# Performance work log

Hardware: AMD Instinct MI355X
Metric: run time of the kernel (lower is better)

Reference implementation:

```python
import jax, jax.numpy as jnp
import numpy as np

UP_TIME = 1440.0
UP_DIST = 40.0
LOC_CNT = 100000
LOC_LEN = 131072
H = 256


def setup_inputs() -> dict:
    key = jax.random.key(0)
    ks = jax.random.split(key, 12)
    stdv = 1.0 / np.sqrt(H)
    u = lambda k, shape: jax.random.uniform(k, shape, jnp.float32, -stdv, stdv)
    return {
        "td_upper": jax.random.uniform(ks[0], (LOC_LEN,), jnp.float32),
        "td_lower": jax.random.uniform(ks[1], (LOC_LEN,), jnp.float32),
        "ld_upper": jax.random.uniform(ks[2], (LOC_LEN,), jnp.float32),
        "ld_lower": jax.random.uniform(ks[3], (LOC_LEN,), jnp.float32),
        "loc": jax.random.randint(ks[4], (LOC_LEN,), 0, LOC_CNT, jnp.int32),
        "hx": jax.random.normal(ks[5], (H, 1), jnp.float32),
        "weight_ih": u(ks[6], (H, H)),
        "weight_th_upper": u(ks[7], (H, H)),
        "weight_th_lower": u(ks[8], (H, H)),
        "weight_sh_upper": u(ks[9], (H, H)),
        "weight_sh_lower": u(ks[10], (H, H)),
        "location_weight": u(ks[11], (LOC_CNT, H)),
    }


def reference(td_upper, td_lower, ld_upper, ld_lower, loc, hx,
              weight_ih, weight_th_upper, weight_th_lower,
              weight_sh_upper, weight_sh_lower, location_weight):
    tu = jnp.clip(td_upper, 0.0, UP_TIME)
    tl = jnp.clip(td_lower, 0.0, UP_TIME)
    lu = jnp.clip(ld_upper, 0.0, UP_DIST)
    ll = jnp.clip(ld_lower, 0.0, UP_DIST)

    e = location_weight[loc]  # [L, H] gathered POI embeddings
    # Ttd[i] @ e[i] = (tu[i]*W_tu@e[i] + tl[i]*W_tl@e[i]) / (tu[i]+tl[i])
    a = jnp.einsum('hk,lk->lh', weight_th_upper, e)
    b = jnp.einsum('hk,lk->lh', weight_th_lower, e)
    t = (tu[:, None] * a + tl[:, None] * b) / (tu + tl)[:, None]  # [L, H]
    # Sld[i] @ t[i]
    c = jnp.einsum('hk,lk->lh', weight_sh_upper, t)
    d = jnp.einsum('hk,lk->lh', weight_sh_lower, t)
    s = (lu[:, None] * c + ll[:, None] * d) / (lu + ll)[:, None]  # [L, H]

    loc_vec = jnp.sum(s, axis=0)[:, None]  # [H, 1]
    usr_vec = weight_ih @ hx               # [H, 1]
    return jax.nn.sigmoid(loc_vec + usr_vec)
```

## Files before the change

### kernel.cpp

```cpp
#include <hip/hip_runtime.h>
#include <math.h>

#define H 256

__global__ __launch_bounds__(256) void strnn_scatter(
    const float* __restrict__ td_u, const float* __restrict__ td_l,
    const float* __restrict__ ld_u, const float* __restrict__ ld_l,
    const int* __restrict__ loc, float* __restrict__ W, int L)
{
    int i = blockIdx.x * blockDim.x + threadIdx.x;
    const int stride = gridDim.x * blockDim.x;
    for (; i < L; i += stride) {
        const float tu = fminf(fmaxf(td_u[i], 0.f), 1440.f);
        const float tl = fminf(fmaxf(td_l[i], 0.f), 1440.f);
        const float lu = fminf(fmaxf(ld_u[i], 0.f), 40.f);
        const float ll = fminf(fmaxf(ld_l[i], 0.f), 40.f);
        const float al = tu / (tu + tl);
        const float be = lu / (lu + ll);
        float* Wr = W + 4 * (size_t)loc[i];
        atomicAdd(Wr + 0, be * al);
        atomicAdd(Wr + 1, be * (1.f - al));
        atomicAdd(Wr + 2, (1.f - be) * al);
        atomicAdd(Wr + 3, (1.f - be) * (1.f - al));
    }
}

__global__ __launch_bounds__(512) void strnn_accum(
    const float* __restrict__ W, const float* __restrict__ table,
    float* __restrict__ v, int R)
{
    __shared__ float s_red[8][4][H];
    const int t    = threadIdx.x;
    const int wave = t >> 6;
    const int lane = t & 63;
    const int nwave = gridDim.x * 8;

    float4 a0 = {0,0,0,0}, a1 = {0,0,0,0}, a2 = {0,0,0,0}, a3 = {0,0,0,0};

    for (int r0 = (blockIdx.x * 8 + wave) * 8; r0 < R; r0 += nwave * 8) {
        float4 wv[8], e[8];
        #pragma unroll
        for (int u = 0; u < 8; ++u) {
            const int r = r0 + u;
            wv[u] = (r < R) ? *(const float4*)(W + 4 * (size_t)r)
                            : make_float4(0.f, 0.f, 0.f, 0.f);
        }
        #pragma unroll
        for (int u = 0; u < 8; ++u) {
            e[u] = make_float4(0.f, 0.f, 0.f, 0.f);
            const float4 w = wv[u];
            if (w.x != 0.f || w.y != 0.f || w.z != 0.f || w.w != 0.f)
                e[u] = *(const float4*)(table + (size_t)(r0 + u) * H + 4 * lane);
        }
        #pragma unroll
        for (int u = 0; u < 8; ++u) {
            const float4 w = wv[u];
            a0.x = fmaf(w.x, e[u].x, a0.x);
            a0.y = fmaf(w.x, e[u].y, a0.y);
            a0.z = fmaf(w.x, e[u].z, a0.z);
            a0.w = fmaf(w.x, e[u].w, a0.w);
            a1.x = fmaf(w.y, e[u].x, a1.x);
            a1.y = fmaf(w.y, e[u].y, a1.y);
            a1.z = fmaf(w.y, e[u].z, a1.z);
            a1.w = fmaf(w.y, e[u].w, a1.w);
            a2.x = fmaf(w.z, e[u].x, a2.x);
            a2.y = fmaf(w.z, e[u].y, a2.y);
            a2.z = fmaf(w.z, e[u].z, a2.z);
            a2.w = fmaf(w.z, e[u].w, a2.w);
            a3.x = fmaf(w.w, e[u].x, a3.x);
            a3.y = fmaf(w.w, e[u].y, a3.y);
            a3.z = fmaf(w.w, e[u].z, a3.z);
            a3.w = fmaf(w.w, e[u].w, a3.w);
        }
    }

    *(float4*)&s_red[wave][0][4 * lane] = a0;
    *(float4*)&s_red[wave][1][4 * lane] = a1;
    *(float4*)&s_red[wave][2][4 * lane] = a2;
    *(float4*)&s_red[wave][3][4 * lane] = a3;
    __syncthreads();
    const int col = t & 255;
    #pragma unroll
    for (int cc = 0; cc < 2; ++cc) {
        const int c = (t >> 8) * 2 + cc;
        float s = 0.f;
        #pragma unroll
        for (int wv_ = 0; wv_ < 8; ++wv_)
            s += s_red[wv_][c][col];
        atomicAdd(&v[c * H + col], s);
    }
}

__global__ __launch_bounds__(256) void strnn_mid(
    const float* __restrict__ Wtu, const float* __restrict__ Wtl,
    const float* __restrict__ Wih, const float* __restrict__ hx,
    const float* __restrict__ v, float* __restrict__ pqu)
{
    const int wave = (blockIdx.x * blockDim.x + threadIdx.x) >> 6;
    const int lane = threadIdx.x & 63;
    const float* v1 = v;
    const float* v2 = v + H;
    const float* v3 = v + 2 * H;
    const float* v4 = v + 3 * H;

    float p = 0.f, q = 0.f, u = 0.f;
    #pragma unroll
    for (int i = 0; i < H; i += 64) {
        const int k = i + lane;
        const float wtu = Wtu[wave * H + k];
        const float wtl = Wtl[wave * H + k];
        p = fmaf(wtu, v1[k], fmaf(wtl, v2[k], p));
        q = fmaf(wtu, v3[k], fmaf(wtl, v4[k], q));
        u = fmaf(Wih[wave * H + k], hx[k], u);
    }
    #pragma unroll
    for (int off = 32; off > 0; off >>= 1) {
        p += __shfl_down(p, off, 64);
        q += __shfl_down(q, off, 64);
        u += __shfl_down(u, off, 64);
    }
    if (lane == 0) {
        pqu[wave]         = p;
        pqu[H + wave]     = q;
        pqu[2 * H + wave] = u;
    }
}

__global__ __launch_bounds__(256) void strnn_out(
    const float* __restrict__ Wsu, const float* __restrict__ Wsl,
    const float* __restrict__ pqu, float* __restrict__ out)
{
    const int wave = (blockIdx.x * blockDim.x + threadIdx.x) >> 6;
    const int lane = threadIdx.x & 63;
    const float* p = pqu;
    const float* q = pqu + H;
    const float* u = pqu + 2 * H;

    float s = 0.f;
    #pragma unroll
    for (int i = 0; i < H; i += 64) {
        const int k = i + lane;
        s = fmaf(Wsu[wave * H + k], p[k], fmaf(Wsl[wave * H + k], q[k], s));
    }
    #pragma unroll
    for (int off = 32; off > 0; off >>= 1)
        s += __shfl_down(s, off, 64);
    if (lane == 0)
        out[wave] = 1.f / (1.f + expf(-(s + u[wave])));
}

extern "C" void kernel_launch(void* const* d_in, const int* in_sizes, int n_in,
                              void* d_out, int out_size, void* d_ws, size_t ws_size,
                              hipStream_t stream) {
    const float* td_u  = (const float*)d_in[0];
    const float* td_l  = (const float*)d_in[1];
    const float* ld_u  = (const float*)d_in[2];
    const float* ld_l  = (const float*)d_in[3];
    const int*   loc   = (const int*)d_in[4];
    const float* hx    = (const float*)d_in[5];
    const float* Wih   = (const float*)d_in[6];
    const float* Wtu   = (const float*)d_in[7];
    const float* Wtl   = (const float*)d_in[8];
    const float* Wsu   = (const float*)d_in[9];
    const float* Wsl   = (const float*)d_in[10];
    const float* table = (const float*)d_in[11];
    const int L = in_sizes[0];
    const int R = in_sizes[11] / H;

    float* W   = (float*)d_ws;
    float* v   = W + (size_t)R * 4;
    float* pqu = v + 4 * H;

    hipMemsetAsync(W, 0, ((size_t)R * 4 + 4 * H) * sizeof(float), stream);

    strnn_scatter<<<512, 256, 0, stream>>>(td_u, td_l, ld_u, ld_l, loc, W, L);
    strnn_accum<<<512, 512, 0, stream>>>(W, table, v, R);
    strnn_mid<<<64, 256, 0, stream>>>(Wtu, Wtl, Wih, hx, v, pqu);
    strnn_out<<<64, 256, 0, stream>>>(Wsu, Wsl, pqu, (float*)d_out);
}
```

Before: 208.7 us.

## Store scatter coefficients as SoA planes and make table gathers branchless

Changes the per-location coefficient buffer from interleaved AoS (4 floats per row) to four padded planes. The accumulate kernel can then load 8 rows of each plane with float4 loads. The table gather becomes branchless: rows with all-zero weights read row 0 instead of being skipped behind a branch. The scatter kernel now launches one thread per element with no grid-stride loop, and the accumulate grid is halved. In exchange, every dead row still issues a load from row 0, though that row should stay in cache, and the atomics spread across four separate planes.

```diff
diff --git a/kernel.cpp b/kernel.cpp
--- a/kernel.cpp
+++ b/kernel.cpp
@@ -6,71 +6,79 @@
 __global__ __launch_bounds__(256) void strnn_scatter(
     const float* __restrict__ td_u, const float* __restrict__ td_l,
     const float* __restrict__ ld_u, const float* __restrict__ ld_l,
-    const int* __restrict__ loc, float* __restrict__ W, int L)
+    const int* __restrict__ loc, float* __restrict__ W, int L, int Rpad)
 {
-    int i = blockIdx.x * blockDim.x + threadIdx.x;
-    const int stride = gridDim.x * blockDim.x;
-    for (; i < L; i += stride) {
-        const float tu = fminf(fmaxf(td_u[i], 0.f), 1440.f);
-        const float tl = fminf(fmaxf(td_l[i], 0.f), 1440.f);
-        const float lu = fminf(fmaxf(ld_u[i], 0.f), 40.f);
-        const float ll = fminf(fmaxf(ld_l[i], 0.f), 40.f);
-        const float al = tu / (tu + tl);
-        const float be = lu / (lu + ll);
-        float* Wr = W + 4 * (size_t)loc[i];
-        atomicAdd(Wr + 0, be * al);
-        atomicAdd(Wr + 1, be * (1.f - al));
-        atomicAdd(Wr + 2, (1.f - be) * al);
-        atomicAdd(Wr + 3, (1.f - be) * (1.f - al));
-    }
+    const int i = blockIdx.x * blockDim.x + threadIdx.x;
+    if (i >= L) return;
+    const float tu = fminf(fmaxf(td_u[i], 0.f), 1440.f);
+    const float tl = fminf(fmaxf(td_l[i], 0.f), 1440.f);
+    const float lu = fminf(fmaxf(ld_u[i], 0.f), 40.f);
+    const float ll = fminf(fmaxf(ld_l[i], 0.f), 40.f);
+    const float al = tu / (tu + tl);
+    const float be = lu / (lu + ll);
+    const int r = loc[i];
+    atomicAdd(W + r,            be * al);
+    atomicAdd(W + Rpad + r,     be * (1.f - al));
+    atomicAdd(W + 2 * Rpad + r, (1.f - be) * al);
+    atomicAdd(W + 3 * Rpad + r, (1.f - be) * (1.f - al));
 }
 
 __global__ __launch_bounds__(512) void strnn_accum(
     const float* __restrict__ W, const float* __restrict__ table,
-    float* __restrict__ v, int R)
+    float* __restrict__ v, int R, int Rpad)
 {
     __shared__ float s_red[8][4][H];
     const int t    = threadIdx.x;
     const int wave = t >> 6;
     const int lane = t & 63;
-    const int nwave = gridDim.x * 8;
+    const float* __restrict__ W0 = W;
+    const float* __restrict__ W1 = W + Rpad;
+    const float* __restrict__ W2 = W + 2 * (size_t)Rpad;
+    const float* __restrict__ W3 = W + 3 * (size_t)Rpad;
 
     float4 a0 = {0,0,0,0}, a1 = {0,0,0,0}, a2 = {0,0,0,0}, a3 = {0,0,0,0};
 
-    for (int r0 = (blockIdx.x * 8 + wave) * 8; r0 < R; r0 += nwave * 8) {
-        float4 wv[8], e[8];
+    const int gw     = blockIdx.x * 8 + wave;
+    const int stride = gridDim.x * 8 * 8;
+
+    for (int r0 = gw * 8; r0 < R; r0 += stride) {
+        float w0[8], w1[8], w2[8], w3[8];
+        *(float4*)&w0[0] = *(const float4*)(W0 + r0);
+        *(float4*)&w0[4] = *(const float4*)(W0 + r0 + 4);
+        *(float4*)&w1[0] = *(const float4*)(W1 + r0);
+        *(float4*)&w1[4] = *(const float4*)(W1 + r0 + 4);
+        *(float4*)&w2[0] = *(const float4*)(W2 + r0);
+        *(float4*)&w2[4] = *(const float4*)(W2 + r0 + 4);
+        *(float4*)&w3[0] = *(const float4*)(W3 + r0);
+        *(float4*)&w3[4] = *(const float4*)(W3 + r0 + 4);
+
+        float4 e[8];
         #pragma unroll
         for (int u = 0; u < 8; ++u) {
             const int r = r0 + u;
-            wv[u] = (r < R) ? *(const float4*)(W + 4 * (size_t)r)
-                            : make_float4(0.f, 0.f, 0.f, 0.f);
+            const bool live = (r < R) &&
+                (w0[u] != 0.f || w1[u] != 0.f || w2[u] != 0.f || w3[u] != 0.f);
+            const size_t roff = live ? (size_t)r * H : (size_t)0;
+            e[u] = *(const float4*)(table + roff + 4 * lane);
         }
         #pragma unroll
         for (int u = 0; u < 8; ++u) {
-            e[u] = make_float4(0.f, 0.f, 0.f, 0.f);
-            const float4 w = wv[u];
-            if (w.x != 0.f || w.y != 0.f || w.z != 0.f || w.w != 0.f)
-                e[u] = *(const float4*)(table + (size_t)(r0 + u) * H + 4 * lane);
-        }
-        #pragma unroll
-        for (int u = 0; u < 8; ++u) {
-            const float4 w = wv[u];
-            a0.x = fmaf(w.x, e[u].x, a0.x);
-            a0.y = fmaf(w.x, e[u].y, a0.y);
-            a0.z = fmaf(w.x, e[u].z, a0.z);
-            a0.w = fmaf(w.x, e[u].w, a0.w);
-            a1.x = fmaf(w.y, e[u].x, a1.x);
-            a1.y = fmaf(w.y, e[u].y, a1.y);
-            a1.z = fmaf(w.y, e[u].z, a1.z);
-            a1.w = fmaf(w.y, e[u].w, a1.w);
-            a2.x = fmaf(w.z, e[u].x, a2.x);
-            a2.y = fmaf(w.z, e[u].y, a2.y);
-            a2.z = fmaf(w.z, e[u].z, a2.z);
-            a2.w = fmaf(w.z, e[u].w, a2.w);
-            a3.x = fmaf(w.w, e[u].x, a3.x);
-            a3.y = fmaf(w.w, e[u].y, a3.y);
-            a3.z = fmaf(w.w, e[u].z, a3.z);
-            a3.w = fmaf(w.w, e[u].w, a3.w);
+            a0.x = fmaf(w0[u], e[u].x, a0.x);
+            a0.y = fmaf(w0[u], e[u].y, a0.y);
+            a0.z = fmaf(w0[u], e[u].z, a0.z);
+            a0.w = fmaf(w0[u], e[u].w, a0.w);
+            a1.x = fmaf(w1[u], e[u].x, a1.x);
+            a1.y = fmaf(w1[u], e[u].y, a1.y);
+            a1.z = fmaf(w1[u], e[u].z, a1.z);
+            a1.w = fmaf(w1[u], e[u].w, a1.w);
+            a2.x = fmaf(w2[u], e[u].x, a2.x);
+            a2.y = fmaf(w2[u], e[u].y, a2.y);
+            a2.z = fmaf(w2[u], e[u].z, a2.z);
+            a2.w = fmaf(w2[u], e[u].w, a2.w);
+            a3.x = fmaf(w3[u], e[u].x, a3.x);
+            a3.y = fmaf(w3[u], e[u].y, a3.y);
+            a3.z = fmaf(w3[u], e[u].z, a3.z);
+            a3.w = fmaf(w3[u], e[u].w, a3.w);
         }
     }
 
@@ -85,8 +93,8 @@
         const int c = (t >> 8) * 2 + cc;
         float s = 0.f;
         #pragma unroll
-        for (int wv_ = 0; wv_ < 8; ++wv_)
-            s += s_red[wv_][c][col];
+        for (int w_ = 0; w_ < 8; ++w_)
+            s += s_red[w_][c][col];
         atomicAdd(&v[c * H + col], s);
     }
 }
@@ -166,15 +174,17 @@
     const float* table = (const float*)d_in[11];
     const int L = in_sizes[0];
     const int R = in_sizes[11] / H;
+    const int Rpad = (R + 7) & ~7;
 
     float* W   = (float*)d_ws;
-    float* v   = W + (size_t)R * 4;
+    float* v   = W + 4 * (size_t)Rpad;
     float* pqu = v + 4 * H;
 
-    hipMemsetAsync(W, 0, ((size_t)R * 4 + 4 * H) * sizeof(float), stream);
+    hipMemsetAsync(W, 0, (4 * (size_t)Rpad + 4 * H) * sizeof(float), stream);
 
-    strnn_scatter<<<512, 256, 0, stream>>>(td_u, td_l, ld_u, ld_l, loc, W, L);
-    strnn_accum<<<512, 512, 0, stream>>>(W, table, v, R);
+    strnn_scatter<<<(L + 255) / 256, 256, 0, stream>>>(
+        td_u, td_l, ld_u, ld_l, loc, W, L, Rpad);
+    strnn_accum<<<256, 512, 0, stream>>>(W, table, v, R, Rpad);
     strnn_mid<<<64, 256, 0, stream>>>(Wtu, Wtl, Wih, hx, v, pqu);
     strnn_out<<<64, 256, 0, stream>>>(Wsu, Wsl, pqu, (float*)d_out);
 }
```

Result: faster. 203.5 us (-2.5%).
